# Performance work log

Hardware: AMD Instinct MI355X
Metric: run time of the kernel (lower is better)

Reference implementation:

```python
import jax, jax.numpy as jnp
import numpy as np

N = 50000
E = 800000
IN_C = 128
HID = 8
OUT_C = 32
HEADS = (4, 4, 4)
NEG_SLOPE = 0.2


def gat_conv(x, src, dst, W, att_src, att_dst, bias, heads, out_c, concat):
    # x: [N, F_in]; W: [F_in, heads*out_c]; att_*: [heads, out_c]; bias: [heads*out_c] or [out_c]
    n = x.shape[0]
    h = (x @ W).reshape(n, heads, out_c)                      # [N, H, C]
    a_src = (h * att_src).sum(-1)                             # [N, H]
    a_dst = (h * att_dst).sum(-1)                             # [N, H]
    e = jax.nn.leaky_relu(a_src[src] + a_dst[dst], NEG_SLOPE)  # [E, H]
    # segment softmax over edges grouped by destination node
    m = jax.ops.segment_max(e, dst, num_segments=n)           # [N, H]
    m = jnp.where(jnp.isfinite(m), m, 0.0)
    p = jnp.exp(e - m[dst])                                   # [E, H]
    s = jax.ops.segment_sum(p, dst, num_segments=n)           # [N, H]
    alpha = p / (s[dst] + 1e-16)                              # [E, H]
    msg = h[src] * alpha[:, :, None]                          # [E, H, C]
    out = jax.ops.segment_sum(msg, dst, num_segments=n)       # [N, H, C]
    out = out.reshape(n, heads * out_c) if concat else out.mean(axis=1)
    return out + bias


def setup_inputs() -> dict:
    key = jax.random.key(0)
    ks = jax.random.split(key, 16)
    x = jax.random.normal(ks[0], (N, IN_C), dtype=jnp.float32)
    edge_index = jax.random.randint(ks[1], (2, E), 0, N, dtype=jnp.int64)
    c1 = HID                       # per-head out of conv1 (8)
    c2 = HID * HEADS[0]            # per-head out of conv2 (32)
    c3 = OUT_C                     # per-head out of conv3 (32)
    in2 = HID * HEADS[0]           # 32
    in3 = HID * HEADS[0] * HEADS[1]  # 128
    sc = 0.1
    return {
        "x": x,
        "edge_index": edge_index,
        "W1": jax.random.normal(ks[2], (IN_C, HEADS[0] * c1), dtype=jnp.float32) * sc,
        "as1": jax.random.normal(ks[3], (HEADS[0], c1), dtype=jnp.float32) * sc,
        "ad1": jax.random.normal(ks[4], (HEADS[0], c1), dtype=jnp.float32) * sc,
        "b1": jnp.zeros((HEADS[0] * c1,), dtype=jnp.float32),
        "W2": jax.random.normal(ks[5], (in2, HEADS[1] * c2), dtype=jnp.float32) * sc,
        "as2": jax.random.normal(ks[6], (HEADS[1], c2), dtype=jnp.float32) * sc,
        "ad2": jax.random.normal(ks[7], (HEADS[1], c2), dtype=jnp.float32) * sc,
        "b2": jnp.zeros((HEADS[1] * c2,), dtype=jnp.float32),
        "W3": jax.random.normal(ks[8], (in3, HEADS[2] * c3), dtype=jnp.float32) * sc,
        "as3": jax.random.normal(ks[9], (HEADS[2], c3), dtype=jnp.float32) * sc,
        "ad3": jax.random.normal(ks[10], (HEADS[2], c3), dtype=jnp.float32) * sc,
        "b3": jnp.zeros((c3,), dtype=jnp.float32),
    }


def reference(x, edge_index, W1, as1, ad1, b1, W2, as2, ad2, b2, W3, as3, ad3, b3):
    src, dst = edge_index[0], edge_index[1]
    h = gat_conv(x, src, dst, W1, as1, ad1, b1, HEADS[0], HID, True)
    h = jax.nn.elu(h)
    h = gat_conv(h, src, dst, W2, as2, ad2, b2, HEADS[1], HID * HEADS[0], True)
    h = jax.nn.elu(h)
    out = gat_conv(h, src, dst, W3, as3, ad3, b3, HEADS[2], OUT_C, False)
    return out
```

## Files before the change

kernel.cpp:

```cpp
#include <hip/hip_runtime.h>
#include <hip/hip_fp16.h>

#define NEG_SLOPE 0.2f

static inline int cdiv(long long a, long long b) { return (int)((a + b - 1) / b); }

typedef _Float16 f16x8 __attribute__((ext_vector_type(8)));
typedef float f32x4 __attribute__((ext_vector_type(4)));

__device__ __forceinline__ float4 f4_add(float4 a, float4 b) {
    return make_float4(a.x + b.x, a.y + b.y, a.z + b.z, a.w + b.w);
}
__device__ __forceinline__ float4 f4_leaky(float4 a) {
    return make_float4(a.x > 0.f ? a.x : NEG_SLOPE * a.x,
                       a.y > 0.f ? a.y : NEG_SLOPE * a.y,
                       a.z > 0.f ? a.z : NEG_SLOPE * a.z,
                       a.w > 0.f ? a.w : NEG_SLOPE * a.w);
}
__device__ __forceinline__ float4 f4_exp(float4 e) {
    return make_float4(__expf(e.x), __expf(e.y), __expf(e.z), __expf(e.w));
}
__device__ __forceinline__ float f4_get(float4 v, int i) {
    return i == 0 ? v.x : i == 1 ? v.y : i == 2 ? v.z : v.w;
}

union h4u {
    float2  f2;
    __half2 h2[2];
};

__global__ void detect_i64_kernel(const void* ei_raw, int E_, int n, int* flag)
{
    if (blockIdx.x == 0 && threadIdx.x == 0) {
        const long long* e64 = (const long long*)ei_raw;
        int cnt = E_ < 512 ? E_ : 512;
        int ok = 1;
        for (int i = 0; i < cnt; i++) {
            long long v = e64[i];
            if (v < 0 || v >= n) { ok = 0; break; }
        }
        *flag = ok;
    }
}

__device__ __forceinline__ void load_sd(const void* ei_raw, int is64, int e, int E_,
                                        int& s, int& d)
{
    if (is64) {
        const long long* p = (const long long*)ei_raw;
        s = (int)p[e];
        d = (int)p[E_ + e];
    } else {
        const int* p = (const int*)ei_raw;
        s = p[e];
        d = p[E_ + e];
    }
}

__global__ __launch_bounds__(256) void cvt_x_kernel(const float* __restrict__ x,
                                                    __half* __restrict__ xh, int total8)
{
    int idx = blockIdx.x * 256 + threadIdx.x;
    if (idx >= total8) return;
    const float4* p = (const float4*)(x) + idx * 2;
    float4 a = p[0], b = p[1];
    f16x8 v = {(_Float16)a.x, (_Float16)a.y, (_Float16)a.z, (_Float16)a.w,
               (_Float16)b.x, (_Float16)b.y, (_Float16)b.z, (_Float16)b.w};
    *(f16x8*)(xh + (size_t)idx * 8) = v;
}

__global__ __launch_bounds__(256) void cvt_w_kernel(const float* __restrict__ W,
                                                    __half* __restrict__ Wt,
                                                    int K, int NOUT)
{
    int idx = blockIdx.x * 256 + threadIdx.x;
    if (idx >= K * NOUT) return;
    int k = idx / NOUT, col = idx % NOUT;
    Wt[col * K + k] = __float2half(W[idx]);
}

__global__ __launch_bounds__(256) void hist_kernel(const void* __restrict__ ei_raw,
                                                   const int* __restrict__ flag,
                                                   int* __restrict__ deg,
                                                   int* __restrict__ s32,
                                                   int* __restrict__ d32,
                                                   int* __restrict__ rank, int E_)
{
    int base = blockIdx.x * 1024 + threadIdx.x;
    int is64 = *flag;
    int sj[4], dj[4], rj[4];
    bool v[4];
#pragma unroll
    for (int j = 0; j < 4; j++) {
        int e = base + j * 256;
        v[j] = e < E_;
        if (v[j]) load_sd(ei_raw, is64, e, E_, sj[j], dj[j]);
    }
#pragma unroll
    for (int j = 0; j < 4; j++) {
        int e = base + j * 256;
        if (v[j]) { s32[e] = sj[j]; d32[e] = dj[j]; }
    }
#pragma unroll
    for (int j = 0; j < 4; j++) {
        if (v[j]) rj[j] = atomicAdd(deg + dj[j], 1);
    }
#pragma unroll
    for (int j = 0; j < 4; j++) {
        int e = base + j * 256;
        if (v[j]) rank[e] = rj[j];
    }
}

__device__ __forceinline__ int wave_incl_scan(int v)
{
    int lane = threadIdx.x & 63;
#pragma unroll
    for (int off = 1; off < 64; off <<= 1) {
        int t = __shfl_up(v, off);
        if (lane >= off) v += t;
    }
    return v;
}

__global__ __launch_bounds__(1024) void scan_part_kernel(const int* __restrict__ deg,
                                                         int* __restrict__ start,
                                                         int* __restrict__ bsum, int n)
{
    __shared__ int wsum[16];
    int i = blockIdx.x * 1024 + threadIdx.x;
    int wid = threadIdx.x >> 6, lane = threadIdx.x & 63;
    int v = (i < n) ? deg[i] : 0;
    int incl = wave_incl_scan(v);
    if (lane == 63) wsum[wid] = incl;
    __syncthreads();
    if (wid == 0) {
        int w = (lane < 16) ? wsum[lane] : 0;
        w = wave_incl_scan(w);
        if (lane < 16) wsum[lane] = w;
    }
    __syncthreads();
    int excl = incl - v + (wid ? wsum[wid - 1] : 0);
    if (i < n) start[i] = excl;
    if (threadIdx.x == 1023) bsum[blockIdx.x] = wsum[15];
}

__global__ __launch_bounds__(1024) void scan_bsum_kernel(int* __restrict__ bsum, int nb)
{
    __shared__ int sh[1024];
    int t = threadIdx.x;
    sh[t] = (t < nb) ? bsum[t] : 0;
    __syncthreads();
    for (int off = 1; off < 1024; off <<= 1) {
        int val = (t >= off) ? sh[t - off] : 0;
        __syncthreads();
        sh[t] += val;
        __syncthreads();
    }
    if (t < nb) bsum[t] = t ? sh[t - 1] : 0;
}

__global__ __launch_bounds__(1024) void scan_add_kernel(const int* __restrict__ deg,
                                                        const int* __restrict__ boffs,
                                                        int* __restrict__ start, int n)
{
    int i = blockIdx.x * 1024 + threadIdx.x;
    if (i >= n) return;
    int v = start[i] + boffs[blockIdx.x];
    start[i] = v;
    if (i == n - 1) start[n] = v + deg[i];
}

__global__ __launch_bounds__(256) void scatter_kernel(const int* __restrict__ s32,
                                                      const int* __restrict__ d32,
                                                      const int* __restrict__ rank,
                                                      const int* __restrict__ start,
                                                      int* __restrict__ sorted_src, int E_)
{
    int base = blockIdx.x * 1024 + threadIdx.x;
    int sj[4], dj[4], rj[4];
    bool v[4];
#pragma unroll
    for (int j = 0; j < 4; j++) {
        int e = base + j * 256;
        v[j] = e < E_;
        sj[j] = v[j] ? s32[e] : 0;
        dj[j] = v[j] ? d32[e] : 0;
        rj[j] = v[j] ? rank[e] : 0;
    }
    int pj[4];
#pragma unroll
    for (int j = 0; j < 4; j++) {
        if (v[j]) pj[j] = start[dj[j]] + rj[j];
    }
#pragma unroll
    for (int j = 0; j < 4; j++) {
        if (v[j]) __builtin_nontemporal_store(sj[j], sorted_src + pj[j]);
    }
}

template <int K, int NOUT>
__global__ __launch_bounds__(256) void gemm_mfma_kernel(
    const __half* __restrict__ xh, const __half* __restrict__ Wt,
    const float* __restrict__ att_s, const float* __restrict__ att_d,
    __half* __restrict__ h, float* __restrict__ a_s, float* __restrict__ a_d, int n)
{
    constexpr int KC = 32;
    constexpr int NT = NOUT / 16;
    constexpr int XP = KC + 8;
    constexpr int HP = NOUT + 8;
    constexpr int C  = NOUT / 4;

    __shared__ _Float16 Xs[64 * XP];
    __shared__ _Float16 Ws[NOUT * XP];
    __shared__ _Float16 Hs[64 * HP];
    __shared__ float As[NOUT], Ad[NOUT];

    const int tid  = threadIdx.x;
    const int nb   = blockIdx.x * 64;
    const int wave = tid >> 6, lane = tid & 63;
    const int m16  = lane & 15, quad = lane >> 4;

    if (tid < NOUT) { As[tid] = att_s[tid]; Ad[tid] = att_d[tid]; }

    f32x4 acc[NT];
#pragma unroll
    for (int t = 0; t < NT; t++) acc[t] = (f32x4){0.f, 0.f, 0.f, 0.f};

    for (int kc = 0; kc < K; kc += KC) {
        {
            int node = tid >> 2, seg = tid & 3;
            int gn = nb + node;
            f16x8 v = {0, 0, 0, 0, 0, 0, 0, 0};
            if (gn < n) v = *(const f16x8*)(xh + (size_t)gn * K + kc + seg * 8);
            *(f16x8*)&Xs[node * XP + seg * 8] = v;
        }
        for (int u = tid; u < NOUT * 4; u += 256) {
            int col = u >> 2, seg = u & 3;
            *(f16x8*)&Ws[col * XP + seg * 8] =
                *(const f16x8*)(Wt + (size_t)col * K + kc + seg * 8);
        }
        __syncthreads();

        f16x8 a = *(const f16x8*)&Xs[(wave * 16 + m16) * XP + quad * 8];
#pragma unroll
        for (int t = 0; t < NT; t++) {
            f16x8 b = *(const f16x8*)&Ws[(t * 16 + m16) * XP + quad * 8];
            acc[t] = __builtin_amdgcn_mfma_f32_16x16x32_f16(a, b, acc[t], 0, 0, 0);
        }
        __syncthreads();
    }

#pragma unroll
    for (int t = 0; t < NT; t++) {
#pragma unroll
        for (int r = 0; r < 4; r++) {
            int row = wave * 16 + quad * 4 + r;
            Hs[row * HP + t * 16 + m16] = (_Float16)acc[t][r];
        }
    }
    __syncthreads();

    for (int u = tid; u < 64 * NOUT / 8; u += 256) {
        int row = u / (NOUT / 8), seg = u % (NOUT / 8);
        int gn = nb + row;
        if (gn < n)
            *(f16x8*)(h + (size_t)gn * NOUT + seg * 8) =
                *(const f16x8*)&Hs[row * HP + seg * 8];
    }

    {
        int node = tid >> 2, head = tid & 3;
        int gn = nb + node;
        const _Float16* hr = &Hs[node * HP + head * C];
        float s1 = 0.f, s2 = 0.f;
#pragma unroll 4
        for (int c = 0; c < C; c++) {
            float v = (float)hr[c];
            s1 += v * As[head * C + c];
            s2 += v * Ad[head * C + c];
        }
        if (gn < n) {
            a_s[gn * 4 + head] = s1;
            a_d[gn * 4 + head] = s2;
        }
    }
}

template <int MODE>
__global__ __launch_bounds__(256) void gat_agg128_kernel(
    const int* __restrict__ start, const int* __restrict__ sorted_src,
    const __half* __restrict__ h, const float* __restrict__ a_s,
    const float* __restrict__ a_d, const float* __restrict__ bias,
    void* __restrict__ out, int n)
{
    constexpr int MAXD = 64;
    __shared__ float  p_sh[8][MAXD * 4];
    __shared__ float4 invs_sh[8];

    int local = threadIdx.x >> 5;
    int q     = threadIdx.x & 31;
    int node  = blockIdx.x * 8 + local;
    bool active = node < n;
    int s0 = 0, s1 = 0;
    if (active) { s0 = start[node]; s1 = start[node + 1]; }
    int deg = s1 - s0;

    const float4* as4 = (const float4*)a_s;
    float4 ad = active ? ((const float4*)a_d)[node] : make_float4(0.f, 0.f, 0.f, 0.f);

    float4 sm = make_float4(0.f, 0.f, 0.f, 0.f);
    for (int i = s0 + q; i < s1; i += 32) {
        int s = sorted_src[i];
        float4 p = f4_exp(f4_leaky(f4_add(as4[s], ad)));
        sm = f4_add(sm, p);
        int j = i - s0;
        if (j < MAXD) ((float4*)&p_sh[local][0])[j] = p;
    }
#pragma unroll
    for (int off = 16; off; off >>= 1) {
        sm.x += __shfl_xor(sm.x, off, 32);
        sm.y += __shfl_xor(sm.y, off, 32);
        sm.z += __shfl_xor(sm.z, off, 32);
        sm.w += __shfl_xor(sm.w, off, 32);
    }
    if (q == 0) {
        invs_sh[local] = make_float4(1.f / (sm.x + 1e-16f), 1.f / (sm.y + 1e-16f),
                                     1.f / (sm.z + 1e-16f), 1.f / (sm.w + 1e-16f));
    }
    __syncthreads();

    int head = q >> 3;
    float invh = f4_get(invs_sh[local], head);
    const float2* __restrict__ h2 = (const float2*)h + q;
    const float* __restrict__ pl = &p_sh[local][0];

    float4 acc = make_float4(0.f, 0.f, 0.f, 0.f);
    if (deg <= MAXD) {
        int i = 0;
        for (; i + 8 <= deg; i += 8) {
            int   sj[8];
            float aj[8];
#pragma unroll
            for (int j = 0; j < 8; j++) sj[j] = sorted_src[s0 + i + j];
#pragma unroll
            for (int j = 0; j < 8; j++) aj[j] = pl[(i + j) * 4 + head] * invh;
            float2 rj[8];
#pragma unroll
            for (int j = 0; j < 8; j++) rj[j] = h2[(size_t)sj[j] * 32];
#pragma unroll
            for (int j = 0; j < 8; j++) {
                h4u u; u.f2 = rj[j];
                float2 lo = __half22float2(u.h2[0]);
                float2 hi = __half22float2(u.h2[1]);
                acc.x += lo.x * aj[j]; acc.y += lo.y * aj[j];
                acc.z += hi.x * aj[j]; acc.w += hi.y * aj[j];
            }
        }
        for (; i < deg; i++) {
            h4u u; u.f2 = h2[(size_t)sorted_src[s0 + i] * 32];
            float a = pl[i * 4 + head] * invh;
            float2 lo = __half22float2(u.h2[0]);
            float2 hi = __half22float2(u.h2[1]);
            acc.x += lo.x * a; acc.y += lo.y * a; acc.z += hi.x * a; acc.w += hi.y * a;
        }
    } else {
        for (int i = s0; i < s1; i++) {
            int s = sorted_src[i];
            float4 p = f4_exp(f4_leaky(f4_add(as4[s], ad)));
            float a = f4_get(p, head) * invh;
            h4u u; u.f2 = h2[(size_t)s * 32];
            float2 lo = __half22float2(u.h2[0]);
            float2 hi = __half22float2(u.h2[1]);
            acc.x += lo.x * a; acc.y += lo.y * a; acc.z += hi.x * a; acc.w += hi.y * a;
        }
    }

    if (MODE == 0) {
        if (active) {
            float4 b4 = ((const float4*)bias)[q];
            float4 v = f4_add(acc, b4);
            v.x = v.x > 0.f ? v.x : (__expf(v.x) - 1.f);
            v.y = v.y > 0.f ? v.y : (__expf(v.y) - 1.f);
            v.z = v.z > 0.f ? v.z : (__expf(v.z) - 1.f);
            v.w = v.w > 0.f ? v.w : (__expf(v.w) - 1.f);
            h4u u;
            u.h2[0] = __floats2half2_rn(v.x, v.y);
            u.h2[1] = __floats2half2_rn(v.z, v.w);
            *(float2*)((__half*)out + (size_t)node * 128 + q * 4) = u.f2;
        }
    } else {
        __shared__ float4 sh4[8][33];
        sh4[local][q] = acc;
        __syncthreads();
        if (q < 8 && active) {
            float4 a = sh4[local][q];
            float4 b = sh4[local][q + 8];
            float4 c = sh4[local][q + 16];
            float4 d = sh4[local][q + 24];
            float4 b4 = ((const float4*)bias)[q];
            float4 r = make_float4(0.25f * (a.x + b.x + c.x + d.x) + b4.x,
                                   0.25f * (a.y + b.y + c.y + d.y) + b4.y,
                                   0.25f * (a.z + b.z + c.z + d.z) + b4.z,
                                   0.25f * (a.w + b.w + c.w + d.w) + b4.w);
            *(float4*)((float*)out + (size_t)node * 32 + q * 4) = r;
        }
    }
}

__global__ __launch_bounds__(256) void gat_agg32_kernel(
    const int* __restrict__ start, const int* __restrict__ sorted_src,
    const __half* __restrict__ h, const float* __restrict__ a_s,
    const float* __restrict__ a_d, const float* __restrict__ bias,
    __half* __restrict__ out, int n)
{
    constexpr int MAXD = 32;
    __shared__ float  p_sh[32][MAXD * 4];
    __shared__ float4 invs_sh[32];

    int local = threadIdx.x >> 3;
    int q     = threadIdx.x & 7;
    int node  = blockIdx.x * 32 + local;
    bool active = node < n;
    int s0 = 0, s1 = 0;
    if (active) { s0 = start[node]; s1 = start[node + 1]; }
    int deg = s1 - s0;

    const float4* as4 = (const float4*)a_s;
    float4 ad = active ? ((const float4*)a_d)[node] : make_float4(0.f, 0.f, 0.f, 0.f);

    float4 sm = make_float4(0.f, 0.f, 0.f, 0.f);
    for (int i = s0 + q; i < s1; i += 8) {
        int s = sorted_src[i];
        float4 p = f4_exp(f4_leaky(f4_add(as4[s], ad)));
        sm = f4_add(sm, p);
        int j = i - s0;
        if (j < MAXD) ((float4*)&p_sh[local][0])[j] = p;
    }
#pragma unroll
    for (int off = 4; off; off >>= 1) {
        sm.x += __shfl_xor(sm.x, off, 8);
        sm.y += __shfl_xor(sm.y, off, 8);
        sm.z += __shfl_xor(sm.z, off, 8);
        sm.w += __shfl_xor(sm.w, off, 8);
    }
    if (q == 0) {
        invs_sh[local] = make_float4(1.f / (sm.x + 1e-16f), 1.f / (sm.y + 1e-16f),
                                     1.f / (sm.z + 1e-16f), 1.f / (sm.w + 1e-16f));
    }
    __syncthreads();

    int head = q >> 1;
    float invh = f4_get(invs_sh[local], head);
    const float2* __restrict__ h2 = (const float2*)h + q;
    const float* __restrict__ pl = &p_sh[local][0];

    float4 acc = make_float4(0.f, 0.f, 0.f, 0.f);
    if (deg <= MAXD) {
        int i = 0;
        for (; i + 8 <= deg; i += 8) {
            int   sj[8];
            float aj[8];
#pragma unroll
            for (int j = 0; j < 8; j++) sj[j] = sorted_src[s0 + i + j];
#pragma unroll
            for (int j = 0; j < 8; j++) aj[j] = pl[(i + j) * 4 + head] * invh;
            float2 rj[8];
#pragma unroll
            for (int j = 0; j < 8; j++) rj[j] = h2[(size_t)sj[j] * 8];
#pragma unroll
            for (int j = 0; j < 8; j++) {
                h4u u; u.f2 = rj[j];
                float2 lo = __half22float2(u.h2[0]);
                float2 hi = __half22float2(u.h2[1]);
                acc.x += lo.x * aj[j]; acc.y += lo.y * aj[j];
                acc.z += hi.x * aj[j]; acc.w += hi.y * aj[j];
            }
        }
        for (; i < deg; i++) {
            h4u u; u.f2 = h2[(size_t)sorted_src[s0 + i] * 8];
            float a = pl[i * 4 + head] * invh;
            float2 lo = __half22float2(u.h2[0]);
            float2 hi = __half22float2(u.h2[1]);
            acc.x += lo.x * a; acc.y += lo.y * a; acc.z += hi.x * a; acc.w += hi.y * a;
        }
    } else {
        for (int i = s0; i < s1; i++) {
            int s = sorted_src[i];
            float4 p = f4_exp(f4_leaky(f4_add(as4[s], ad)));
            float a = f4_get(p, head) * invh;
            h4u u; u.f2 = h2[(size_t)s * 8];
            float2 lo = __half22float2(u.h2[0]);
            float2 hi = __half22float2(u.h2[1]);
            acc.x += lo.x * a; acc.y += lo.y * a; acc.z += hi.x * a; acc.w += hi.y * a;
        }
    }

    if (active) {
        float4 b4 = ((const float4*)bias)[q];
        float4 v = f4_add(acc, b4);
        v.x = v.x > 0.f ? v.x : (__expf(v.x) - 1.f);
        v.y = v.y > 0.f ? v.y : (__expf(v.y) - 1.f);
        v.z = v.z > 0.f ? v.z : (__expf(v.z) - 1.f);
        v.w = v.w > 0.f ? v.w : (__expf(v.w) - 1.f);
        h4u u;
        u.h2[0] = __floats2half2_rn(v.x, v.y);
        u.h2[1] = __floats2half2_rn(v.z, v.w);
        *(float2*)(out + (size_t)node * 32 + q * 4) = u.f2;
    }
}


extern "C" void kernel_launch(void* const* d_in, const int* in_sizes, int n_in,
                              void* d_out, int out_size, void* d_ws, size_t ws_size,
                              hipStream_t stream)
{
    const float* x   = (const float*)d_in[0];
    const void*  ei  = d_in[1];
    const float* W1  = (const float*)d_in[2];
    const float* as1 = (const float*)d_in[3];
    const float* ad1 = (const float*)d_in[4];
    const float* b1  = (const float*)d_in[5];
    const float* W2  = (const float*)d_in[6];
    const float* as2 = (const float*)d_in[7];
    const float* ad2 = (const float*)d_in[8];
    const float* b2  = (const float*)d_in[9];
    const float* W3  = (const float*)d_in[10];
    const float* as3 = (const float*)d_in[11];
    const float* ad3 = (const float*)d_in[12];
    const float* b3  = (const float*)d_in[13];
    float* out = (float*)d_out;

    const int N_ = in_sizes[0] / 128;
    const int E_ = in_sizes[1] / 2;

    char* ws = (char*)d_ws;
    size_t off = 0;
    auto alloc = [&](size_t nbytes) -> void* {
        void* p = ws + off;
        off += (nbytes + 255) & ~(size_t)255;
        return p;
    };
    __half* xh        = (__half*)alloc((size_t)N_ * 128 * 2);
    __half* h         = (__half*)alloc((size_t)N_ * 128 * 2);
    __half* x2h       = (__half*)alloc((size_t)N_ * 32 * 2);
    __half* x3h       = (__half*)alloc((size_t)N_ * 128 * 2);
    __half* Wt1       = (__half*)alloc(128 * 32 * 2);
    __half* Wt2       = (__half*)alloc(32 * 128 * 2);
    __half* Wt3       = (__half*)alloc(128 * 128 * 2);
    float* asrc       = (float*)alloc((size_t)N_ * 4 * 4);
    float* adst       = (float*)alloc((size_t)N_ * 4 * 4);
    int*   deg        = (int*)alloc((size_t)N_ * 4);
    int*   start      = (int*)alloc((size_t)(N_ + 1) * 4);
    int*   sorted_src = (int*)alloc((size_t)E_ * 4);
    int*   s32        = (int*)alloc((size_t)E_ * 4);
    int*   d32        = (int*)alloc((size_t)E_ * 4);
    int*   rank       = (int*)alloc((size_t)E_ * 4);
    int*   bsum       = (int*)alloc(4096);
    int*   flag       = (int*)alloc(256);

    const int gN8  = cdiv(N_, 8);
    const int gN32 = cdiv(N_, 32);
    const int gN64 = cdiv(N_, 64);
    const int nSB  = cdiv(N_, 1024);

    cvt_x_kernel<<<cdiv((long long)N_ * 16, 256), 256, 0, stream>>>(x, xh, N_ * 16);
    cvt_w_kernel<<<cdiv(128 * 32, 256), 256, 0, stream>>>(W1, Wt1, 128, 32);
    cvt_w_kernel<<<cdiv(32 * 128, 256), 256, 0, stream>>>(W2, Wt2, 32, 128);
    cvt_w_kernel<<<cdiv(128 * 128, 256), 256, 0, stream>>>(W3, Wt3, 128, 128);

    detect_i64_kernel<<<1, 1, 0, stream>>>(ei, E_, N_, flag);
    hipMemsetAsync(deg, 0, (size_t)N_ * 4, stream);
    hist_kernel<<<cdiv(E_, 1024), 256, 0, stream>>>(ei, flag, deg, s32, d32, rank, E_);
    scan_part_kernel<<<nSB, 1024, 0, stream>>>(deg, start, bsum, N_);
    scan_bsum_kernel<<<1, 1024, 0, stream>>>(bsum, nSB);
    scan_add_kernel<<<nSB, 1024, 0, stream>>>(deg, bsum, start, N_);
    scatter_kernel<<<cdiv(E_, 1024), 256, 0, stream>>>(s32, d32, rank, start,
                                                       sorted_src, E_);

    gemm_mfma_kernel<128, 32><<<gN64, 256, 0, stream>>>(xh, Wt1, as1, ad1, h,
                                                        asrc, adst, N_);
    gat_agg32_kernel<<<gN32, 256, 0, stream>>>(start, sorted_src, h, asrc, adst, b1,
                                               x2h, N_);

    gemm_mfma_kernel<32, 128><<<gN64, 256, 0, stream>>>(x2h, Wt2, as2, ad2, h,
                                                        asrc, adst, N_);
    gat_agg128_kernel<0><<<gN8, 256, 0, stream>>>(start, sorted_src, h, asrc, adst, b2,
                                                  x3h, N_);

    gemm_mfma_kernel<128, 128><<<gN64, 256, 0, stream>>>(x3h, Wt3, as3, ad3, h,
                                                         asrc, adst, N_);
    gat_agg128_kernel<1><<<gN8, 256, 0, stream>>>(start, sorted_src, h, asrc, adst, b3,
                                                  out, N_);
}
```

Before: 323.6 us.

## Fuse prep kernels, fold fp32-to-fp16 x conversion into first GEMM, drop bsum scan

Merges the int64 detection, degree zeroing and the three weight conversions into one prep kernel, replacing several small launches and a memset. The first GEMM now reads fp32 x directly and converts it while loading, which removes the separate cvt_x pass and its 12.8MB fp16 intermediate. The single-block bsum scan kernel is dropped; each scan_add block instead sums the preceding block totals serially in one thread, which is cheap with about 49 blocks. The trade-off is that the first GEMM reads twice as many bytes per x tile.

```diff
diff --git a/kernel.cpp b/kernel.cpp
--- a/kernel.cpp
+++ b/kernel.cpp
@@ -28,20 +28,6 @@
     float2  f2;
     __half2 h2[2];
 };
-
-__global__ void detect_i64_kernel(const void* ei_raw, int E_, int n, int* flag)
-{
-    if (blockIdx.x == 0 && threadIdx.x == 0) {
-        const long long* e64 = (const long long*)ei_raw;
-        int cnt = E_ < 512 ? E_ : 512;
-        int ok = 1;
-        for (int i = 0; i < cnt; i++) {
-            long long v = e64[i];
-            if (v < 0 || v >= n) { ok = 0; break; }
-        }
-        *flag = ok;
-    }
-}
 
 __device__ __forceinline__ void load_sd(const void* ei_raw, int is64, int e, int E_,
                                         int& s, int& d)
@@ -57,26 +43,45 @@
     }
 }
 
-__global__ __launch_bounds__(256) void cvt_x_kernel(const float* __restrict__ x,
-                                                    __half* __restrict__ xh, int total8)
+__global__ __launch_bounds__(256) void prep_kernel(
+    const void* __restrict__ ei, int E_, int n, int* __restrict__ flag,
+    int* __restrict__ deg,
+    const float* __restrict__ W1, __half* __restrict__ Wt1,
+    const float* __restrict__ W2, __half* __restrict__ Wt2,
+    const float* __restrict__ W3, __half* __restrict__ Wt3)
 {
     int idx = blockIdx.x * 256 + threadIdx.x;
-    if (idx >= total8) return;
-    const float4* p = (const float4*)(x) + idx * 2;
-    float4 a = p[0], b = p[1];
-    f16x8 v = {(_Float16)a.x, (_Float16)a.y, (_Float16)a.z, (_Float16)a.w,
-               (_Float16)b.x, (_Float16)b.y, (_Float16)b.z, (_Float16)b.w};
-    *(f16x8*)(xh + (size_t)idx * 8) = v;
-}
-
-__global__ __launch_bounds__(256) void cvt_w_kernel(const float* __restrict__ W,
-                                                    __half* __restrict__ Wt,
-                                                    int K, int NOUT)
-{
-    int idx = blockIdx.x * 256 + threadIdx.x;
-    if (idx >= K * NOUT) return;
-    int k = idx / NOUT, col = idx % NOUT;
-    Wt[col * K + k] = __float2half(W[idx]);
+
+    if (blockIdx.x == 0) {
+        __shared__ int bad;
+        if (threadIdx.x == 0) bad = 0;
+        __syncthreads();
+        const long long* e64 = (const long long*)ei;
+        int cnt = E_ < 512 ? E_ : 512;
+        bool ok = true;
+        for (int i = threadIdx.x; i < cnt; i += 256) {
+            long long v = e64[i];
+            if (v < 0 || v >= n) ok = false;
+        }
+        if (!ok) atomicAdd(&bad, 1);
+        __syncthreads();
+        if (threadIdx.x == 0) *flag = (bad == 0) ? 1 : 0;
+    }
+
+    if (idx < n) deg[idx] = 0;
+
+    if (idx < 128 * 32) {
+        int k = idx / 32, c = idx % 32;
+        Wt1[c * 128 + k] = __float2half(W1[idx]);
+    }
+    if (idx < 32 * 128) {
+        int k = idx / 128, c = idx % 128;
+        Wt2[c * 32 + k] = __float2half(W2[idx]);
+    }
+    if (idx < 128 * 128) {
+        int k = idx / 128, c = idx % 128;
+        Wt3[c * 128 + k] = __float2half(W3[idx]);
+    }
 }
 
 __global__ __launch_bounds__(256) void hist_kernel(const void* __restrict__ ei_raw,
@@ -145,28 +150,20 @@
     if (threadIdx.x == 1023) bsum[blockIdx.x] = wsum[15];
 }
 
-__global__ __launch_bounds__(1024) void scan_bsum_kernel(int* __restrict__ bsum, int nb)
-{
-    __shared__ int sh[1024];
-    int t = threadIdx.x;
-    sh[t] = (t < nb) ? bsum[t] : 0;
+__global__ __launch_bounds__(1024) void scan_add_kernel(const int* __restrict__ deg,
+                                                        const int* __restrict__ bsum,
+                                                        int* __restrict__ start, int n)
+{
+    __shared__ int off_sh;
+    if (threadIdx.x == 0) {
+        int s = 0;
+        for (int j = 0; j < blockIdx.x; j++) s += bsum[j];
+        off_sh = s;
+    }
     __syncthreads();
-    for (int off = 1; off < 1024; off <<= 1) {
-        int val = (t >= off) ? sh[t - off] : 0;
-        __syncthreads();
-        sh[t] += val;
-        __syncthreads();
-    }
-    if (t < nb) bsum[t] = t ? sh[t - 1] : 0;
-}
-
-__global__ __launch_bounds__(1024) void scan_add_kernel(const int* __restrict__ deg,
-                                                        const int* __restrict__ boffs,
-                                                        int* __restrict__ start, int n)
-{
     int i = blockIdx.x * 1024 + threadIdx.x;
     if (i >= n) return;
-    int v = start[i] + boffs[blockIdx.x];
+    int v = start[i] + off_sh;
     start[i] = v;
     if (i == n - 1) start[n] = v + deg[i];
 }
@@ -199,9 +196,9 @@
     }
 }
 
-template <int K, int NOUT>
+template <int K, int NOUT, int A16>
 __global__ __launch_bounds__(256) void gemm_mfma_kernel(
-    const __half* __restrict__ xh, const __half* __restrict__ Wt,
+    const void* __restrict__ xin, const __half* __restrict__ Wt,
     const float* __restrict__ att_s, const float* __restrict__ att_d,
     __half* __restrict__ h, float* __restrict__ a_s, float* __restrict__ a_d, int n)
 {
@@ -232,7 +229,19 @@
             int node = tid >> 2, seg = tid & 3;
             int gn = nb + node;
             f16x8 v = {0, 0, 0, 0, 0, 0, 0, 0};
-            if (gn < n) v = *(const f16x8*)(xh + (size_t)gn * K + kc + seg * 8);
+            if (gn < n) {
+                if (A16) {
+                    v = *(const f16x8*)((const __half*)xin + (size_t)gn * K + kc +
+                                        seg * 8);
+                } else {
+                    const float4* p =
+                        (const float4*)((const float*)xin + (size_t)gn * K + kc + seg * 8);
+                    float4 a = p[0], b = p[1];
+                    v = (f16x8){(_Float16)a.x, (_Float16)a.y, (_Float16)a.z,
+                                (_Float16)a.w, (_Float16)b.x, (_Float16)b.y,
+                                (_Float16)b.z, (_Float16)b.w};
+                }
+            }
             *(f16x8*)&Xs[node * XP + seg * 8] = v;
         }
         for (int u = tid; u < NOUT * 4; u += 256) {
@@ -541,7 +550,6 @@
         off += (nbytes + 255) & ~(size_t)255;
         return p;
     };
-    __half* xh        = (__half*)alloc((size_t)N_ * 128 * 2);
     __half* h         = (__half*)alloc((size_t)N_ * 128 * 2);
     __half* x2h       = (__half*)alloc((size_t)N_ * 32 * 2);
     __half* x3h       = (__half*)alloc((size_t)N_ * 128 * 2);
@@ -563,33 +571,28 @@
     const int gN32 = cdiv(N_, 32);
     const int gN64 = cdiv(N_, 64);
     const int nSB  = cdiv(N_, 1024);
-
-    cvt_x_kernel<<<cdiv((long long)N_ * 16, 256), 256, 0, stream>>>(x, xh, N_ * 16);
-    cvt_w_kernel<<<cdiv(128 * 32, 256), 256, 0, stream>>>(W1, Wt1, 128, 32);
-    cvt_w_kernel<<<cdiv(32 * 128, 256), 256, 0, stream>>>(W2, Wt2, 32, 128);
-    cvt_w_kernel<<<cdiv(128 * 128, 256), 256, 0, stream>>>(W3, Wt3, 128, 128);
-
-    detect_i64_kernel<<<1, 1, 0, stream>>>(ei, E_, N_, flag);
-    hipMemsetAsync(deg, 0, (size_t)N_ * 4, stream);
+    int prepWork = N_ > 128 * 128 ? N_ : 128 * 128;
+
+    prep_kernel<<<cdiv(prepWork, 256), 256, 0, stream>>>(ei, E_, N_, flag, deg,
+                                                         W1, Wt1, W2, Wt2, W3, Wt3);
     hist_kernel<<<cdiv(E_, 1024), 256, 0, stream>>>(ei, flag, deg, s32, d32, rank, E_);
     scan_part_kernel<<<nSB, 1024, 0, stream>>>(deg, start, bsum, N_);
-    scan_bsum_kernel<<<1, 1024, 0, stream>>>(bsum, nSB);
     scan_add_kernel<<<nSB, 1024, 0, stream>>>(deg, bsum, start, N_);
     scatter_kernel<<<cdiv(E_, 1024), 256, 0, stream>>>(s32, d32, rank, start,
                                                        sorted_src, E_);
 
-    gemm_mfma_kernel<128, 32><<<gN64, 256, 0, stream>>>(xh, Wt1, as1, ad1, h,
-                                                        asrc, adst, N_);
+    gemm_mfma_kernel<128, 32, 0><<<gN64, 256, 0, stream>>>(x, Wt1, as1, ad1, h,
+                                                           asrc, adst, N_);
     gat_agg32_kernel<<<gN32, 256, 0, stream>>>(start, sorted_src, h, asrc, adst, b1,
                                                x2h, N_);
 
-    gemm_mfma_kernel<32, 128><<<gN64, 256, 0, stream>>>(x2h, Wt2, as2, ad2, h,
-                                                        asrc, adst, N_);
+    gemm_mfma_kernel<32, 128, 1><<<gN64, 256, 0, stream>>>(x2h, Wt2, as2, ad2, h,
+                                                           asrc, adst, N_);
     gat_agg128_kernel<0><<<gN8, 256, 0, stream>>>(start, sorted_src, h, asrc, adst, b2,
                                                   x3h, N_);
 
-    gemm_mfma_kernel<128, 128><<<gN64, 256, 0, stream>>>(x3h, Wt3, as3, ad3, h,
-                                                         asrc, adst, N_);
+    gemm_mfma_kernel<128, 128, 1><<<gN64, 256, 0, stream>>>(x3h, Wt3, as3, ad3, h,
+                                                            asrc, adst, N_);
     gat_agg128_kernel<1><<<gN8, 256, 0, stream>>>(start, sorted_src, h, asrc, adst, b3,
                                                   out, N_);
 }
```

New measurement: 313.0 us. -3.3%, faster.
